# Optimization experiments

Measured on AMD Instinct MI355X. Metric: run time of the kernel, lower is better.

Reference implementation:

```python
import jax, jax.numpy as jnp
import numpy as np

# dims
B, L, IN, H, OUT = 2, 2048, 128, 512, 64
NL, ED, N, DR, K = 2, 1024, 16, 32, 4  # n_layers, d_inner=2*H, d_state, dt_rank=ceil(H/16), d_conv


def setup_inputs() -> dict:
    key = jax.random.key(0)
    ks = jax.random.split(key, 18)
    r = lambda k, s: 0.05 * jax.random.normal(k, s, dtype=jnp.float32)
    return {
        "x": jax.random.normal(ks[0], (B, L, IN), dtype=jnp.float32),
        # LiquidNet proj (in_dim -> hidden -> hidden)
        "p_Wi": r(ks[1], (IN, H)), "p_bi": r(ks[2], (H,)), "p_bh": r(ks[3], (H,)),
        "p_Wo": r(ks[4], (H, H)), "p_bo": r(ks[5], (H,)),
        # Mamba layers (stacked over layer axis)
        "m_norm_w": jnp.ones((NL, H), jnp.float32),
        "m_in_W": r(ks[6], (NL, H, 2 * ED)),
        "m_conv_w": r(ks[7], (NL, ED, K)), "m_conv_b": r(ks[8], (NL, ED)),
        "m_xproj_W": r(ks[9], (NL, ED, DR + 2 * N)),
        "m_dt_W": r(ks[10], (NL, DR, ED)), "m_dt_b": r(ks[11], (NL, ED)),
        "m_A_log": jnp.tile(jnp.log(jnp.arange(1, N + 1, dtype=jnp.float32)), (NL, ED, 1)),
        "m_D": jnp.ones((NL, ED), jnp.float32),
        "m_out_W": r(ks[12], (NL, ED, H)),
        # LiquidNet dense (hidden -> out_dim -> out_dim)
        "d_Wi": r(ks[13], (H, OUT)), "d_bi": r(ks[14], (OUT,)), "d_bh": r(ks[15], (OUT,)),
        "d_Wo": r(ks[16], (OUT, OUT)), "d_bo": r(ks[17], (OUT,)),
    }


def _rmsnorm(x, w, eps=1e-5):
    return x * jax.lax.rsqrt(jnp.mean(x * x, axis=-1, keepdims=True) + eps) * w


def _liquid(x, Wi, bi, bh, Wo, bo):
    # liquid cell with zero initial hidden state: h = tanh(i2h(x) + h2h(0))
    h = jnp.tanh(x @ Wi + bi + bh)
    return h @ Wo + bo


def _causal_conv(x, w, b):
    # x: [B, L, ED]; depthwise causal conv with kernel K
    xt = x.transpose(0, 2, 1)  # [B, ED, L]
    y = jax.lax.conv_general_dilated(xt, w[:, None, :], (1,), [(K - 1, 0)],
                                     dimension_numbers=('NCH', 'OIH', 'NCH'),
                                     feature_group_count=ED)
    return (y + b[None, :, None]).transpose(0, 2, 1)


def _ssm(xc, delta, Bm, Cm, A, D):
    # xc/delta: [B,L,ED]; Bm/Cm: [B,L,N]; A: [ED,N]; D: [ED]
    deltaA = jnp.exp(delta[..., None] * A)                              # [B,L,ED,N]
    deltaBx = delta[..., None] * Bm[:, :, None, :] * xc[..., None]      # [B,L,ED,N]

    def step(h, t):
        dA, dBx, Ct = t
        h = dA * h + dBx
        return h, jnp.einsum('bdn,bn->bd', h, Ct)

    h0 = jnp.zeros((xc.shape[0], ED, N), xc.dtype)
    _, ys = jax.lax.scan(step, h0, (deltaA.transpose(1, 0, 2, 3),
                                    deltaBx.transpose(1, 0, 2, 3),
                                    Cm.transpose(1, 0, 2)))
    return ys.transpose(1, 0, 2) + D * xc


def _mamba_block(x, norm_w, in_W, conv_w, conv_b, xproj_W, dt_W, dt_b, A_log, D, out_W):
    xn = _rmsnorm(x, norm_w)
    xz = xn @ in_W                       # [B,L,2*ED]
    xc, z = jnp.split(xz, 2, axis=-1)
    xc = jax.nn.silu(_causal_conv(xc, conv_w, conv_b))
    dbl = xc @ xproj_W                   # [B,L,DR+2N]
    dt, Bm, Cm = dbl[..., :DR], dbl[..., DR:DR + N], dbl[..., DR + N:]
    delta = jax.nn.softplus(dt @ dt_W + dt_b)
    y = _ssm(xc, delta, Bm, Cm, -jnp.exp(A_log), D)
    y = y * jax.nn.silu(z)
    return y @ out_W


def reference(x, p_Wi, p_bi, p_bh, p_Wo, p_bo,
              m_norm_w, m_in_W, m_conv_w, m_conv_b, m_xproj_W, m_dt_W, m_dt_b,
              m_A_log, m_D, m_out_W,
              d_Wi, d_bi, d_bh, d_Wo, d_bo):
    out = _liquid(x, p_Wi, p_bi, p_bh, p_Wo, p_bo)
    for l in range(NL):  # residual Mamba blocks
        out = out + _mamba_block(out, m_norm_w[l], m_in_W[l], m_conv_w[l], m_conv_b[l],
                                 m_xproj_W[l], m_dt_W[l], m_dt_b[l], m_A_log[l], m_D[l], m_out_W[l])
    out = _liquid(out, d_Wi, d_bi, d_bh, d_Wo, d_bo)
    out = out - jnp.tanh(out)  # Tanhshrink
    return out.reshape(-1)
```

## Files before the change

### kernel.cpp

```cpp
#include <hip/hip_runtime.h>
#include <hip/hip_bf16.h>
#include <cstdint>
#include <cstddef>

#define B_   2
#define L_   2048
#define IN_  128
#define H_   512
#define OUT_ 64
#define NL_  2
#define ED_  1024
#define N_   16
#define DR_  32
#define K_   4

static constexpr int M_TOK = B_ * L_;
static constexpr int SEG   = 64;
static constexpr int TS    = L_ / SEG;

typedef __attribute__((ext_vector_type(8))) short bhalf8;
typedef __attribute__((ext_vector_type(4))) float floatx4;

__device__ __forceinline__ void gld_lds16(const ushort* g, ushort* l)
{
    __builtin_amdgcn_global_load_lds(
        (const __attribute__((address_space(1))) unsigned int*)g,
        (__attribute__((address_space(3))) unsigned int*)l, 16, 0, 0);
}

template<int BM, int BN, int BK, int EPI, bool DUAL>
__global__ __launch_bounds__(256)
void mfma_gemm(const ushort* __restrict__ A, int lda,
               const ushort* Bt, int ldb,
               const ushort* Bt2, float* C2,
               const float* __restrict__ b1, const float* __restrict__ b2,
               float* C, __hip_bfloat16* Cb, int ldc,
               int M, int N, int kc)
{
    __shared__ __align__(16) ushort As[BM * BK];
    __shared__ __align__(16) ushort Bs[BN * BK];

    const int tid  = threadIdx.x;
    const int bm   = blockIdx.x * BM, bn = blockIdx.y * BN;
    int kz = 0, kbeg = 0;
    if (DUAL) {
        if (blockIdx.z) { Bt = Bt2; C = C2; }
    } else {
        kz = blockIdx.z; kbeg = kz * kc;
    }
    const int lane = tid & 63, wave = tid >> 6;
    const int wr = wave >> 1, wc = wave & 1;
    constexpr int WM = BM / 2, WN = BN / 2;
    constexpr int FM = WM / 16, FN = WN / 16;
    const int fr = lane & 15, fg = lane >> 4;

    constexpr int ACH = BM * BK / 512;
    constexpr int BCH = BN * BK / 512;
    constexpr int RPC = 512 / BK;
    constexpr int LPR = BK / 8;
    const int sr = lane / LPR;
    const int sc = (lane % LPR) * 8;

    floatx4 acc[FM][FN] = {};

    for (int k0 = kbeg; k0 < kbeg + kc; k0 += BK) {
        #pragma unroll
        for (int i = 0; i < ACH / 4; ++i) {
            const int ci = wave * (ACH / 4) + i;
            const int r  = ci * RPC + sr;
            gld_lds16(&A[(size_t)(bm + r) * lda + k0 + sc], &As[ci * 512]);
        }
        #pragma unroll
        for (int i = 0; i < BCH / 4; ++i) {
            const int ci = wave * (BCH / 4) + i;
            const int r  = ci * RPC + sr;
            gld_lds16(&Bt[(size_t)(bn + r) * ldb + k0 + sc], &Bs[ci * 512]);
        }
        __syncthreads();
        #pragma unroll
        for (int kk = 0; kk < BK; kk += 32) {
            bhalf8 fa[FM], fb[FN];
            #pragma unroll
            for (int m = 0; m < FM; ++m)
                fa[m] = *reinterpret_cast<const bhalf8*>(
                    &As[(wr * WM + m * 16 + fr) * BK + kk + fg * 8]);
            #pragma unroll
            for (int n = 0; n < FN; ++n)
                fb[n] = *reinterpret_cast<const bhalf8*>(
                    &Bs[(wc * WN + n * 16 + fr) * BK + kk + fg * 8]);
            #pragma unroll
            for (int m = 0; m < FM; ++m)
                #pragma unroll
                for (int n = 0; n < FN; ++n)
                    acc[m][n] = __builtin_amdgcn_mfma_f32_16x16x32_bf16(
                        fa[m], fb[n], acc[m][n], 0, 0, 0);
        }
        __syncthreads();
    }

    #pragma unroll
    for (int m = 0; m < FM; ++m) {
        #pragma unroll
        for (int n = 0; n < FN; ++n) {
            const int row0 = bm + wr * WM + m * 16 + fg * 4;
            const int col  = bn + wc * WN + n * 16 + fr;
            #pragma unroll
            for (int r = 0; r < 4; ++r) {
                float v = acc[m][n][r];
                const int row = row0 + r;
                if (EPI == 0) {
                    C[(size_t)row * ldc + col] = v;
                } else if (EPI == 1) {
                    C[(size_t)row * ldc + col] += v;
                } else if (EPI == 2) {
                    Cb[(size_t)row * ldc + col] =
                        __float2bfloat16(tanhf(v + b1[col] + b2[col]));
                } else if (EPI == 3) {
                    C[(size_t)row * ldc + col] = v + b1[col];
                } else if (EPI == 4) {
                    C[(size_t)kz * M * N + (size_t)row * N + col] = v;
                } else if (EPI == 5) {
                    const float w = v + b1[col];
                    C[(size_t)row * ldc + col] = w - tanhf(w);
                } else if (EPI == 6) {
                    const float w = v + b1[col];
                    C[(size_t)row * ldc + col] =
                        fmaxf(w, 0.0f) + log1pf(expf(-fabsf(w)));
                }
            }
        }
    }
}

template<int NP, int ACT, bool B1, bool B2, int OUTMODE>
__global__ __launch_bounds__(256)
void reduce_part_k(const float* __restrict__ P, const float* __restrict__ b1,
                   const float* __restrict__ b2, float* __restrict__ Of,
                   __hip_bfloat16* __restrict__ Ob, int MN, int Ncols)
{
    const int i = blockIdx.x * 256 + threadIdx.x;
    float s = 0.0f;
    #pragma unroll
    for (int z = 0; z < NP; ++z) s += P[(size_t)z * MN + i];
    const int col = i & (Ncols - 1);
    if (B1) s += b1[col];
    if (B2) s += b2[col];
    if (ACT == 1) s = tanhf(s);
    if (OUTMODE == 0 || OUTMODE == 2) Of[i] = s;
    if (OUTMODE == 1 || OUTMODE == 2) Ob[i] = __float2bfloat16(s);
}

__global__ __launch_bounds__(256)
void transpose_bf16_k(const float* __restrict__ W, __hip_bfloat16* __restrict__ Wt,
                      int K, int N)
{
    __shared__ float t[32][33];
    const int k0 = blockIdx.x * 32, n0 = blockIdx.y * 32;
    const int c = threadIdx.x & 31, r4 = threadIdx.x >> 5;
    #pragma unroll
    for (int i = 0; i < 4; ++i) {
        int r = r4 + i * 8;
        t[r][c] = W[(size_t)(k0 + r) * N + n0 + c];
    }
    __syncthreads();
    #pragma unroll
    for (int i = 0; i < 4; ++i) {
        int r = r4 + i * 8;
        Wt[(size_t)(n0 + r) * K + k0 + c] = __float2bfloat16(t[c][r]);
    }
}

__global__ __launch_bounds__(256)
void cvt_bf16_k(const float* __restrict__ in, __hip_bfloat16* __restrict__ out, int n)
{
    const int i = blockIdx.x * 256 + threadIdx.x;
    if (i < n) out[i] = __float2bfloat16(in[i]);
}

__global__ __launch_bounds__(256)
void rmsnorm_k(const float* __restrict__ x, const float* __restrict__ w,
               __hip_bfloat16* __restrict__ o)
{
    const int row = blockIdx.x;
    const int tid = threadIdx.x;
    const float* xr = x + (size_t)row * H_;
    float v0 = xr[tid], v1 = xr[tid + 256];
    float s = v0 * v0 + v1 * v1;
    #pragma unroll
    for (int off = 32; off > 0; off >>= 1) s += __shfl_down(s, off, 64);
    __shared__ float ps[4];
    __shared__ float scale_s;
    const int wave = tid >> 6, lane = tid & 63;
    if (lane == 0) ps[wave] = s;
    __syncthreads();
    if (tid == 0) {
        float tot = ps[0] + ps[1] + ps[2] + ps[3];
        scale_s = rsqrtf(tot * (1.0f / H_) + 1e-5f);
    }
    __syncthreads();
    const float sc = scale_s;
    o[(size_t)row * H_ + tid]       = __float2bfloat16(v0 * sc * w[tid]);
    o[(size_t)row * H_ + tid + 256] = __float2bfloat16(v1 * sc * w[tid + 256]);
}

__global__ __launch_bounds__(256)
void conv_silu_k(const float* __restrict__ xcr, const float* __restrict__ cw,
                 const float* __restrict__ cb, float* __restrict__ xc,
                 __hip_bfloat16* __restrict__ xcb)
{
    const int idx = blockIdx.x * 256 + threadIdx.x;
    const int d = idx & (ED_ - 1);
    const int t = (idx >> 10) & (L_ - 1);
    const int b = idx >> 21;
    const size_t base = (size_t)(b * L_ + t) * ED_ + d;
    float4 w = *reinterpret_cast<const float4*>(&cw[d * 4]);
    float acc = cb[d];
    acc += w.w * xcr[base];
    if (t >= 1) acc += w.z * xcr[base - 1 * ED_];
    if (t >= 2) acc += w.y * xcr[base - 2 * ED_];
    if (t >= 3) acc += w.x * xcr[base - 3 * ED_];
    const float s = acc / (1.0f + __expf(-acc));
    xc[base] = s;
    xcb[base] = __float2bfloat16(s);
}

template<bool P3>
__global__ __launch_bounds__(256)
void ssm_scan_k(const float* __restrict__ delta,
                const float* __restrict__ xc,
                const float* __restrict__ dbl,
                const float* __restrict__ zbuf,
                const float* __restrict__ A_log,
                const float* __restrict__ Dv,
                float* __restrict__ hend, float* __restrict__ pprod,
                const float* __restrict__ hinit,
                __hip_bfloat16* __restrict__ ybuf)
{
    __shared__ float bc[TS][32];
    const int bx   = blockIdx.x;
    const int seg  = bx & (SEG - 1);
    const int dblk = (bx >> 6) & 3;
    const int b    = bx >> 8;
    const int tid  = threadIdx.x;
    const int d    = dblk * 256 + tid;
    const size_t row0 = (size_t)(b * L_ + seg * TS);

    #pragma unroll
    for (int e = 0; e < (TS * 32) / 256; ++e) {
        int lin = tid + e * 256;
        bc[lin >> 5][lin & 31] = dbl[(row0 + (lin >> 5)) * 64 + 32 + (lin & 31)];
    }
    __syncthreads();

    float Av[N_];
    #pragma unroll
    for (int n = 0; n < N_; ++n) Av[n] = -expf(A_log[d * N_ + n]);

    float dv[TS], xv[TS];
    #pragma unroll
    for (int tt = 0; tt < TS; ++tt) dv[tt] = delta[(row0 + tt) * ED_ + d];
    #pragma unroll
    for (int tt = 0; tt < TS; ++tt) xv[tt] = xc[(row0 + tt) * ED_ + d];

    float h[N_], P[N_];
    if (P3) {
        #pragma unroll
        for (int n = 0; n < N_; ++n)
            h[n] = hinit[((size_t)(b * SEG + seg) * N_ + n) * ED_ + d];
    } else {
        #pragma unroll
        for (int n = 0; n < N_; ++n) { h[n] = 0.0f; P[n] = 1.0f; }
    }
    const float Dd = P3 ? Dv[d] : 0.0f;

    #pragma unroll
    for (int tt = 0; tt < TS; ++tt) {
        const float dvt = dv[tt];
        const float dx  = dvt * xv[tt];
        float ysum = 0.0f;
        #pragma unroll
        for (int n = 0; n < N_; ++n) {
            const float dA = __expf(dvt * Av[n]);
            h[n] = fmaf(dA, h[n], dx * bc[tt][n]);
            if (!P3) P[n] *= dA;
            else     ysum = fmaf(h[n], bc[tt][16 + n], ysum);
        }
        if (P3) {
            const float zv = zbuf[(row0 + tt) * ED_ + d];
            const float sz = zv / (1.0f + __expf(-zv));
            ybuf[(row0 + tt) * ED_ + d] =
                __float2bfloat16((ysum + Dd * xv[tt]) * sz);
        }
    }

    if (!P3) {
        #pragma unroll
        for (int n = 0; n < N_; ++n) {
            const size_t o = ((size_t)(b * SEG + seg) * N_ + n) * ED_ + d;
            hend[o]  = h[n];
            pprod[o] = P[n];
        }
    }
}

__global__ __launch_bounds__(256)
void ssm_combine_k(const float* __restrict__ hend, const float* __restrict__ pprod,
                   float* __restrict__ hinit)
{
    const int gid = blockIdx.x * 256 + threadIdx.x;
    const int d = gid & (ED_ - 1);
    const int n = (gid >> 10) & (N_ - 1);
    const int b = gid >> 14;
    size_t o = ((size_t)(b * SEG) * N_ + n) * ED_ + d;
    const size_t stride = (size_t)N_ * ED_;
    float h = 0.0f;
    #pragma unroll 8
    for (int s = 0; s < SEG; ++s) {
        hinit[o] = h;
        h = fmaf(pprod[o], h, hend[o]);
        o += stride;
    }
}

extern "C" void kernel_launch(void* const* d_in, const int* in_sizes, int n_in,
                              void* d_out, int out_size, void* d_ws, size_t ws_size,
                              hipStream_t stream)
{
    const float* x      = (const float*)d_in[0];
    const float* p_Wi   = (const float*)d_in[1];
    const float* p_bi   = (const float*)d_in[2];
    const float* p_bh   = (const float*)d_in[3];
    const float* p_Wo   = (const float*)d_in[4];
    const float* p_bo   = (const float*)d_in[5];
    const float* m_norm = (const float*)d_in[6];
    const float* m_inW  = (const float*)d_in[7];
    const float* m_cw   = (const float*)d_in[8];
    const float* m_cb   = (const float*)d_in[9];
    const float* m_xpW  = (const float*)d_in[10];
    const float* m_dtW  = (const float*)d_in[11];
    const float* m_dtb  = (const float*)d_in[12];
    const float* m_Alog = (const float*)d_in[13];
    const float* m_D    = (const float*)d_in[14];
    const float* m_outW = (const float*)d_in[15];
    const float* d_Wi   = (const float*)d_in[16];
    const float* d_bi   = (const float*)d_in[17];
    const float* d_bh   = (const float*)d_in[18];
    const float* d_Wo   = (const float*)d_in[19];
    const float* d_bo   = (const float*)d_in[20];
    float* out_f = (float*)d_out;
    float* ws = (float*)d_ws;

    float* OUT   = ws;
    float* XCR   = ws + 2097152;
    float* Z     = ws + 6291456;
    float* XC    = ws + 10485760;
    float* DBL   = ws + 14680064;
    float* DELTA = ws + 14942208;
    float* HINIT = ws + 19136512;
    float* BF    = ws + 21233664;
    float* WT    = ws + 23330816;
    float* DBLF  = ws + 25184256;

    float* HEND   = XCR;
    float* PPROD  = XCR + 2097152;
    float* CPARTX = DELTA;
    float* CPART2 = XCR;
    __hip_bfloat16* Xb   = (__hip_bfloat16*)BF;
    __hip_bfloat16* H1b  = (__hip_bfloat16*)(BF + 262144);
    __hip_bfloat16* XNb  = (__hip_bfloat16*)BF;
    __hip_bfloat16* XCb  = (__hip_bfloat16*)BF;
    __hip_bfloat16* YB   = (__hip_bfloat16*)BF;
    __hip_bfloat16* H2b  = (__hip_bfloat16*)BF;
    __hip_bfloat16* OUTb = (__hip_bfloat16*)XC;
    __hip_bfloat16* DBLb = (__hip_bfloat16*)DBLF;

    __hip_bfloat16* WTu     = (__hip_bfloat16*)WT;
    __hip_bfloat16* T_pWi   = WTu;
    __hip_bfloat16* T_pWo   = WTu + 65536;
    __hip_bfloat16* T_inW0  = WTu + 327680;
    __hip_bfloat16* T_inW1  = WTu + 1376256;
    __hip_bfloat16* T_xpW0  = WTu + 2424832;
    __hip_bfloat16* T_xpW1  = WTu + 2490368;
    __hip_bfloat16* T_outW0 = WTu + 2555904;
    __hip_bfloat16* T_outW1 = WTu + 3080192;
    __hip_bfloat16* T_dWi   = WTu + 3604480;
    __hip_bfloat16* T_dtW0  = WTu + 3637248;
    __hip_bfloat16* T_dtW1  = WTu + 3670016;
    __hip_bfloat16* T_dWo   = WTu + 3702784;

    const dim3 blk(256);

    cvt_bf16_k<<<dim3(2048), blk, 0, stream>>>(x, Xb, M_TOK * IN_);
    transpose_bf16_k<<<dim3(4, 16), blk, 0, stream>>>(p_Wi, T_pWi, IN_, H_);
    transpose_bf16_k<<<dim3(16, 16), blk, 0, stream>>>(p_Wo, T_pWo, H_, H_);
    transpose_bf16_k<<<dim3(16, 64), blk, 0, stream>>>(m_inW, T_inW0, H_, 2 * ED_);
    transpose_bf16_k<<<dim3(16, 64), blk, 0, stream>>>(m_inW + (size_t)H_ * 2 * ED_, T_inW1, H_, 2 * ED_);
    transpose_bf16_k<<<dim3(32, 2), blk, 0, stream>>>(m_xpW, T_xpW0, ED_, 64);
    transpose_bf16_k<<<dim3(32, 2), blk, 0, stream>>>(m_xpW + (size_t)ED_ * 64, T_xpW1, ED_, 64);
    transpose_bf16_k<<<dim3(32, 16), blk, 0, stream>>>(m_outW, T_outW0, ED_, H_);
    transpose_bf16_k<<<dim3(32, 16), blk, 0, stream>>>(m_outW + (size_t)ED_ * H_, T_outW1, ED_, H_);
    transpose_bf16_k<<<dim3(16, 2), blk, 0, stream>>>(d_Wi, T_dWi, H_, OUT_);
    transpose_bf16_k<<<dim3(1, 32), blk, 0, stream>>>(m_dtW, T_dtW0, DR_, ED_);
    transpose_bf16_k<<<dim3(1, 32), blk, 0, stream>>>(m_dtW + DR_ * ED_, T_dtW1, DR_, ED_);
    transpose_bf16_k<<<dim3(2, 2), blk, 0, stream>>>(d_Wo, T_dWo, OUT_, OUT_);

    mfma_gemm<128, 64, 64, 2, false><<<dim3(32, 8), blk, 0, stream>>>(
        (const ushort*)Xb, IN_, (const ushort*)T_pWi, IN_, nullptr, nullptr,
        p_bi, p_bh, nullptr, H1b, H_, M_TOK, H_, IN_);
    mfma_gemm<128, 64, 64, 3, false><<<dim3(32, 8), blk, 0, stream>>>(
        (const ushort*)H1b, H_, (const ushort*)T_pWo, H_, nullptr, nullptr,
        p_bo, nullptr, OUT, nullptr, H_, M_TOK, H_, H_);

    for (int l = 0; l < NL_; ++l) {
        const float* nw   = m_norm + l * H_;
        const float* cw   = m_cw   + l * ED_ * K_;
        const float* cb   = m_cb   + l * ED_;
        const float* dtb  = m_dtb  + l * ED_;
        const float* Alog = m_Alog + l * ED_ * N_;
        const float* Dv   = m_D    + l * ED_;
        const __hip_bfloat16* TinW  = l ? T_inW1  : T_inW0;
        const __hip_bfloat16* TxpW  = l ? T_xpW1  : T_xpW0;
        const __hip_bfloat16* ToutW = l ? T_outW1 : T_outW0;
        const __hip_bfloat16* TdtW  = l ? T_dtW1  : T_dtW0;

        rmsnorm_k<<<dim3(M_TOK), blk, 0, stream>>>(OUT, nw, XNb);
        mfma_gemm<128, 128, 64, 0, true><<<dim3(32, 8, 2), blk, 0, stream>>>(
            (const ushort*)XNb, H_, (const ushort*)TinW, H_,
            (const ushort*)(TinW + (size_t)ED_ * H_), Z,
            nullptr, nullptr, XCR, nullptr, ED_, M_TOK, ED_, H_);
        conv_silu_k<<<dim3(M_TOK * ED_ / 256), blk, 0, stream>>>(XCR, cw, cb, XC, XCb);
        mfma_gemm<128, 64, 64, 4, false><<<dim3(32, 1, 8), blk, 0, stream>>>(
            (const ushort*)XCb, ED_, (const ushort*)TxpW, ED_, nullptr, nullptr,
            nullptr, nullptr, CPARTX, nullptr, 64, M_TOK, 64, ED_ / 8);
        reduce_part_k<8, 0, false, false, 2><<<dim3(1024), blk, 0, stream>>>(
            CPARTX, nullptr, nullptr, DBL, DBLb, M_TOK * 64, 64);
        mfma_gemm<128, 64, 32, 6, false><<<dim3(32, 16), blk, 0, stream>>>(
            (const ushort*)DBLb, 64, (const ushort*)TdtW, DR_, nullptr, nullptr,
            dtb, nullptr, DELTA, nullptr, ED_, M_TOK, ED_, DR_);
        ssm_scan_k<false><<<dim3(512), blk, 0, stream>>>(
            DELTA, XC, DBL, nullptr, Alog, nullptr, HEND, PPROD, nullptr, nullptr);
        ssm_combine_k<<<dim3(128), blk, 0, stream>>>(HEND, PPROD, HINIT);
        ssm_scan_k<true><<<dim3(512), blk, 0, stream>>>(
            DELTA, XC, DBL, Z, Alog, Dv, nullptr, nullptr, HINIT, YB);
        mfma_gemm<128, 64, 64, 1, false><<<dim3(32, 8), blk, 0, stream>>>(
            (const ushort*)YB, ED_, (const ushort*)ToutW, ED_, nullptr, nullptr,
            nullptr, nullptr, OUT, nullptr, H_, M_TOK, H_, ED_);
    }

    cvt_bf16_k<<<dim3(8192), blk, 0, stream>>>(OUT, OUTb, M_TOK * H_);
    mfma_gemm<128, 64, 64, 4, false><<<dim3(32, 1, 8), blk, 0, stream>>>(
        (const ushort*)OUTb, H_, (const ushort*)T_dWi, H_, nullptr, nullptr,
        nullptr, nullptr, CPART2, nullptr, 64, M_TOK, 64, H_ / 8);
    reduce_part_k<8, 1, true, true, 1><<<dim3(1024), blk, 0, stream>>>(
        CPART2, d_bi, d_bh, nullptr, H2b, M_TOK * 64, 64);
    mfma_gemm<128, 64, 64, 5, false><<<dim3(32, 1), blk, 0, stream>>>(
        (const ushort*)H2b, OUT_, (const ushort*)T_dWo, OUT_, nullptr, nullptr,
        d_bo, nullptr, out_f, nullptr, OUT_, M_TOK, OUT_, OUT_);
}
```

Before: 358.4 us.

## Merge prep kernels, vectorize conv, split SSM state across lanes, fuse bf16 cast

Merges the input conversion and thirteen weight-transpose launches into one prep kernel. Vectorizes the causal conv+SiLU kernel to four channels per thread. Restructures the SSM scan so four lanes share each channel, each holding four states, with delta and xc staged in LDS and y reduced by shuffles; this quadruples the block count and lowers register pressure. The final out-projection writes the bf16 copy in its epilogue, removing the separate conversion kernel.

```diff
diff --git a/kernel.cpp b/kernel.cpp
--- a/kernel.cpp
+++ b/kernel.cpp
@@ -20,6 +20,12 @@
 
 typedef __attribute__((ext_vector_type(8))) short bhalf8;
 typedef __attribute__((ext_vector_type(4))) float floatx4;
+
+__device__ __forceinline__ ushort bf16bits(float f)
+{
+    __hip_bfloat16 h = __float2bfloat16(f);
+    return *reinterpret_cast<ushort*>(&h);
+}
 
 __device__ __forceinline__ void gld_lds16(const ushort* g, ushort* l)
 {
@@ -126,6 +132,11 @@
                     const float w = v + b1[col];
                     C[(size_t)row * ldc + col] =
                         fmaxf(w, 0.0f) + log1pf(expf(-fabsf(w)));
+                } else if (EPI == 7) {
+                    float* cp = C + (size_t)row * ldc + col;
+                    const float w = *cp + v;
+                    *cp = w;
+                    Cb[(size_t)row * ldc + col] = __float2bfloat16(w);
                 }
             }
         }
@@ -150,32 +161,66 @@
     if (OUTMODE == 1 || OUTMODE == 2) Ob[i] = __float2bfloat16(s);
 }
 
-__global__ __launch_bounds__(256)
-void transpose_bf16_k(const float* __restrict__ W, __hip_bfloat16* __restrict__ Wt,
-                      int K, int N)
+__device__ __forceinline__ void tr32(float (*t)[33],
+                                     const float* __restrict__ W,
+                                     __hip_bfloat16* __restrict__ Wt,
+                                     int K, int N, int local, int gx, int tid)
+{
+    const int kx = local % gx, ny = local / gx;
+    const int k0 = kx * 32, n0 = ny * 32;
+    const int c = tid & 31, r4 = tid >> 5;
+    #pragma unroll
+    for (int i = 0; i < 4; ++i) {
+        const int rr = r4 + i * 8;
+        t[rr][c] = W[(size_t)(k0 + rr) * N + n0 + c];
+    }
+    __syncthreads();
+    #pragma unroll
+    for (int i = 0; i < 4; ++i) {
+        const int rr = r4 + i * 8;
+        Wt[(size_t)(n0 + rr) * K + k0 + c] = __float2bfloat16(t[c][rr]);
+    }
+}
+
+__global__ __launch_bounds__(256)
+void prep_k(const float* __restrict__ x, __hip_bfloat16* __restrict__ Xb,
+            const float* pWi, __hip_bfloat16* TpWi,
+            const float* pWo, __hip_bfloat16* TpWo,
+            const float* inW, __hip_bfloat16* TinW0, __hip_bfloat16* TinW1,
+            const float* xpW, __hip_bfloat16* TxpW0, __hip_bfloat16* TxpW1,
+            const float* outW, __hip_bfloat16* ToutW0, __hip_bfloat16* ToutW1,
+            const float* dWi, __hip_bfloat16* TdWi,
+            const float* dtW, __hip_bfloat16* TdtW0, __hip_bfloat16* TdtW1,
+            const float* dWo, __hip_bfloat16* TdWo)
 {
     __shared__ float t[32][33];
-    const int k0 = blockIdx.x * 32, n0 = blockIdx.y * 32;
-    const int c = threadIdx.x & 31, r4 = threadIdx.x >> 5;
-    #pragma unroll
-    for (int i = 0; i < 4; ++i) {
-        int r = r4 + i * 8;
-        t[r][c] = W[(size_t)(k0 + r) * N + n0 + c];
-    }
-    __syncthreads();
-    #pragma unroll
-    for (int i = 0; i < 4; ++i) {
-        int r = r4 + i * 8;
-        Wt[(size_t)(n0 + r) * K + k0 + c] = __float2bfloat16(t[c][r]);
-    }
-}
-
-__global__ __launch_bounds__(256)
-void cvt_bf16_k(const float* __restrict__ in, __hip_bfloat16* __restrict__ out, int n)
-{
-    const int i = blockIdx.x * 256 + threadIdx.x;
-    if (i < n) out[i] = __float2bfloat16(in[i]);
-}
+    const int tid = threadIdx.x;
+    int r = blockIdx.x;
+
+    if (r < 512) {
+        const int i = (r * 256 + tid) * 4;
+        const float4 v = *reinterpret_cast<const float4*>(&x[i]);
+        ushort4 u;
+        u.x = bf16bits(v.x); u.y = bf16bits(v.y);
+        u.z = bf16bits(v.z); u.w = bf16bits(v.w);
+        *reinterpret_cast<ushort4*>(&Xb[i]) = u;
+        return;
+    }
+    r -= 512;
+    if (r < 64)   { tr32(t, pWi, TpWi, IN_, H_, r, 4, tid); return; }   r -= 64;
+    if (r < 256)  { tr32(t, pWo, TpWo, H_, H_, r, 16, tid); return; }   r -= 256;
+    if (r < 1024) { tr32(t, inW, TinW0, H_, 2 * ED_, r, 16, tid); return; } r -= 1024;
+    if (r < 1024) { tr32(t, inW + (size_t)H_ * 2 * ED_, TinW1, H_, 2 * ED_, r, 16, tid); return; } r -= 1024;
+    if (r < 64)   { tr32(t, xpW, TxpW0, ED_, 64, r, 32, tid); return; } r -= 64;
+    if (r < 64)   { tr32(t, xpW + (size_t)ED_ * 64, TxpW1, ED_, 64, r, 32, tid); return; } r -= 64;
+    if (r < 512)  { tr32(t, outW, ToutW0, ED_, H_, r, 32, tid); return; } r -= 512;
+    if (r < 512)  { tr32(t, outW + (size_t)ED_ * H_, ToutW1, ED_, H_, r, 32, tid); return; } r -= 512;
+    if (r < 32)   { tr32(t, dWi, TdWi, H_, OUT_, r, 16, tid); return; } r -= 32;
+    if (r < 32)   { tr32(t, dtW, TdtW0, DR_, ED_, r, 1, tid); return; } r -= 32;
+    if (r < 32)   { tr32(t, dtW + DR_ * ED_, TdtW1, DR_, ED_, r, 1, tid); return; } r -= 32;
+    tr32(t, dWo, TdWo, OUT_, OUT_, r, 2, tid);
+}
+static constexpr int PREP_BLOCKS = 512 + 64 + 256 + 1024 + 1024 + 64 + 64 + 512 + 512 + 32 + 32 + 32 + 4;
 
 __global__ __launch_bounds__(256)
 void rmsnorm_k(const float* __restrict__ x, const float* __restrict__ w,
@@ -209,19 +254,34 @@
                  __hip_bfloat16* __restrict__ xcb)
 {
     const int idx = blockIdx.x * 256 + threadIdx.x;
-    const int d = idx & (ED_ - 1);
-    const int t = (idx >> 10) & (L_ - 1);
-    const int b = idx >> 21;
-    const size_t base = (size_t)(b * L_ + t) * ED_ + d;
-    float4 w = *reinterpret_cast<const float4*>(&cw[d * 4]);
-    float acc = cb[d];
-    acc += w.w * xcr[base];
-    if (t >= 1) acc += w.z * xcr[base - 1 * ED_];
-    if (t >= 2) acc += w.y * xcr[base - 2 * ED_];
-    if (t >= 3) acc += w.x * xcr[base - 3 * ED_];
-    const float s = acc / (1.0f + __expf(-acc));
-    xc[base] = s;
-    xcb[base] = __float2bfloat16(s);
+    const int d4 = (idx & (ED_ / 4 - 1)) * 4;
+    const int t  = (idx >> 8) & (L_ - 1);
+    const int b  = idx >> 19;
+    const size_t base = (size_t)(b * L_ + t) * ED_ + d4;
+
+    float4 x0 = *reinterpret_cast<const float4*>(&xcr[base]);
+    float4 x1 = {}, x2 = {}, x3 = {};
+    if (t >= 1) x1 = *reinterpret_cast<const float4*>(&xcr[base - 1 * ED_]);
+    if (t >= 2) x2 = *reinterpret_cast<const float4*>(&xcr[base - 2 * ED_]);
+    if (t >= 3) x3 = *reinterpret_cast<const float4*>(&xcr[base - 3 * ED_]);
+    const float4 bias = *reinterpret_cast<const float4*>(&cb[d4]);
+
+    float4 out;
+    ushort4 outb;
+    #pragma unroll
+    for (int j = 0; j < 4; ++j) {
+        const float4 w = *reinterpret_cast<const float4*>(&cw[(d4 + j) * 4]);
+        float acc = (&bias.x)[j];
+        acc += w.w * (&x0.x)[j];
+        acc += w.z * (&x1.x)[j];
+        acc += w.y * (&x2.x)[j];
+        acc += w.x * (&x3.x)[j];
+        const float s = acc / (1.0f + __expf(-acc));
+        (&out.x)[j] = s;
+        (&outb.x)[j] = bf16bits(s);
+    }
+    *reinterpret_cast<float4*>(&xc[base]) = out;
+    *reinterpret_cast<ushort4*>(&xcb[base]) = outb;
 }
 
 template<bool P3>
@@ -236,69 +296,83 @@
                 const float* __restrict__ hinit,
                 __hip_bfloat16* __restrict__ ybuf)
 {
+    __shared__ float sdl[TS][64];
+    __shared__ float sxc[TS][64];
     __shared__ float bc[TS][32];
     const int bx   = blockIdx.x;
     const int seg  = bx & (SEG - 1);
-    const int dblk = (bx >> 6) & 3;
-    const int b    = bx >> 8;
+    const int dblk = (bx >> 6) & 15;
+    const int b    = bx >> 10;
     const int tid  = threadIdx.x;
-    const int d    = dblk * 256 + tid;
+    const int dl   = tid >> 2;
+    const int ng   = tid & 3;
+    const int d    = dblk * 64 + dl;
+    const int dbase = dblk * 64;
     const size_t row0 = (size_t)(b * L_ + seg * TS);
 
     #pragma unroll
-    for (int e = 0; e < (TS * 32) / 256; ++e) {
-        int lin = tid + e * 256;
+    for (int e = 0; e < 8; ++e) {
+        const int lin = tid + e * 256;
+        sdl[lin >> 6][lin & 63] = delta[(row0 + (lin >> 6)) * ED_ + dbase + (lin & 63)];
+    }
+    #pragma unroll
+    for (int e = 0; e < 8; ++e) {
+        const int lin = tid + e * 256;
+        sxc[lin >> 6][lin & 63] = xc[(row0 + (lin >> 6)) * ED_ + dbase + (lin & 63)];
+    }
+    #pragma unroll
+    for (int e = 0; e < 4; ++e) {
+        const int lin = tid + e * 256;
         bc[lin >> 5][lin & 31] = dbl[(row0 + (lin >> 5)) * 64 + 32 + (lin & 31)];
     }
+
+    float Av[4];
+    #pragma unroll
+    for (int i = 0; i < 4; ++i) Av[i] = -expf(A_log[d * N_ + ng * 4 + i]);
+
+    float h[4], P[4];
+    if (P3) {
+        #pragma unroll
+        for (int i = 0; i < 4; ++i)
+            h[i] = hinit[((size_t)(b * SEG + seg) * N_ + ng * 4 + i) * ED_ + d];
+    } else {
+        #pragma unroll
+        for (int i = 0; i < 4; ++i) { h[i] = 0.0f; P[i] = 1.0f; }
+    }
+    const float Dd = P3 ? Dv[d] : 0.0f;
     __syncthreads();
 
-    float Av[N_];
-    #pragma unroll
-    for (int n = 0; n < N_; ++n) Av[n] = -expf(A_log[d * N_ + n]);
-
-    float dv[TS], xv[TS];
-    #pragma unroll
-    for (int tt = 0; tt < TS; ++tt) dv[tt] = delta[(row0 + tt) * ED_ + d];
-    #pragma unroll
-    for (int tt = 0; tt < TS; ++tt) xv[tt] = xc[(row0 + tt) * ED_ + d];
-
-    float h[N_], P[N_];
-    if (P3) {
-        #pragma unroll
-        for (int n = 0; n < N_; ++n)
-            h[n] = hinit[((size_t)(b * SEG + seg) * N_ + n) * ED_ + d];
-    } else {
-        #pragma unroll
-        for (int n = 0; n < N_; ++n) { h[n] = 0.0f; P[n] = 1.0f; }
-    }
-    const float Dd = P3 ? Dv[d] : 0.0f;
-
-    #pragma unroll
-    for (int tt = 0; tt < TS; ++tt) {
-        const float dvt = dv[tt];
-        const float dx  = dvt * xv[tt];
+    #pragma unroll
+    for (int t = 0; t < TS; ++t) {
+        const float dvt = sdl[t][dl];
+        const float xvt = sxc[t][dl];
+        const float dx  = dvt * xvt;
         float ysum = 0.0f;
         #pragma unroll
-        for (int n = 0; n < N_; ++n) {
-            const float dA = __expf(dvt * Av[n]);
-            h[n] = fmaf(dA, h[n], dx * bc[tt][n]);
-            if (!P3) P[n] *= dA;
-            else     ysum = fmaf(h[n], bc[tt][16 + n], ysum);
+        for (int i = 0; i < 4; ++i) {
+            const float dA = __expf(dvt * Av[i]);
+            h[i] = fmaf(dA, h[i], dx * bc[t][ng * 4 + i]);
+            if (!P3) P[i] *= dA;
+            else     ysum = fmaf(h[i], bc[t][16 + ng * 4 + i], ysum);
         }
         if (P3) {
-            const float zv = zbuf[(row0 + tt) * ED_ + d];
-            const float sz = zv / (1.0f + __expf(-zv));
-            ybuf[(row0 + tt) * ED_ + d] =
-                __float2bfloat16((ysum + Dd * xv[tt]) * sz);
+            float y2 = ysum + __shfl_xor(ysum, 1, 64);
+            float y4 = y2 + __shfl_xor(y2, 2, 64);
+            if (ng == 0) {
+                const float zv = zbuf[(row0 + t) * ED_ + d];
+                const float sz = zv / (1.0f + __expf(-zv));
+                ybuf[(row0 + t) * ED_ + d] =
+                    __float2bfloat16((y4 + Dd * xvt) * sz);
+            }
         }
     }
 
     if (!P3) {
         #pragma unroll
-        for (int n = 0; n < N_; ++n) {
-            const size_t o = ((size_t)(b * SEG + seg) * N_ + n) * ED_ + d;
-            hend[o]  = h[n];
-            pprod[o] = P[n];
+        for (int i = 0; i < 4; ++i) {
+            const size_t o = ((size_t)(b * SEG + seg) * N_ + ng * 4 + i) * ED_ + d;
+            hend[o]  = h[i];
+            pprod[o] = P[i];
         }
     }
 }
@@ -390,19 +464,10 @@
 
     const dim3 blk(256);
 
-    cvt_bf16_k<<<dim3(2048), blk, 0, stream>>>(x, Xb, M_TOK * IN_);
-    transpose_bf16_k<<<dim3(4, 16), blk, 0, stream>>>(p_Wi, T_pWi, IN_, H_);
-    transpose_bf16_k<<<dim3(16, 16), blk, 0, stream>>>(p_Wo, T_pWo, H_, H_);
-    transpose_bf16_k<<<dim3(16, 64), blk, 0, stream>>>(m_inW, T_inW0, H_, 2 * ED_);
-    transpose_bf16_k<<<dim3(16, 64), blk, 0, stream>>>(m_inW + (size_t)H_ * 2 * ED_, T_inW1, H_, 2 * ED_);
-    transpose_bf16_k<<<dim3(32, 2), blk, 0, stream>>>(m_xpW, T_xpW0, ED_, 64);
-    transpose_bf16_k<<<dim3(32, 2), blk, 0, stream>>>(m_xpW + (size_t)ED_ * 64, T_xpW1, ED_, 64);
-    transpose_bf16_k<<<dim3(32, 16), blk, 0, stream>>>(m_outW, T_outW0, ED_, H_);
-    transpose_bf16_k<<<dim3(32, 16), blk, 0, stream>>>(m_outW + (size_t)ED_ * H_, T_outW1, ED_, H_);
-    transpose_bf16_k<<<dim3(16, 2), blk, 0, stream>>>(d_Wi, T_dWi, H_, OUT_);
-    transpose_bf16_k<<<dim3(1, 32), blk, 0, stream>>>(m_dtW, T_dtW0, DR_, ED_);
-    transpose_bf16_k<<<dim3(1, 32), blk, 0, stream>>>(m_dtW + DR_ * ED_, T_dtW1, DR_, ED_);
-    transpose_bf16_k<<<dim3(2, 2), blk, 0, stream>>>(d_Wo, T_dWo, OUT_, OUT_);
+    prep_k<<<dim3(PREP_BLOCKS), blk, 0, stream>>>(
+        x, Xb, p_Wi, T_pWi, p_Wo, T_pWo, m_inW, T_inW0, T_inW1,
+        m_xpW, T_xpW0, T_xpW1, m_outW, T_outW0, T_outW1,
+        d_Wi, T_dWi, m_dtW, T_dtW0, T_dtW1, d_Wo, T_dWo);
 
     mfma_gemm<128, 64, 64, 2, false><<<dim3(32, 8), blk, 0, stream>>>(
         (const ushort*)Xb, IN_, (const ushort*)T_pWi, IN_, nullptr, nullptr,
@@ -428,7 +493,7 @@
             (const ushort*)XNb, H_, (const ushort*)TinW, H_,
             (const ushort*)(TinW + (size_t)ED_ * H_), Z,
             nullptr, nullptr, XCR, nullptr, ED_, M_TOK, ED_, H_);
-        conv_silu_k<<<dim3(M_TOK * ED_ / 256), blk, 0, stream>>>(XCR, cw, cb, XC, XCb);
+        conv_silu_k<<<dim3(M_TOK * ED_ / 4 / 256), blk, 0, stream>>>(XCR, cw, cb, XC, XCb);
         mfma_gemm<128, 64, 64, 4, false><<<dim3(32, 1, 8), blk, 0, stream>>>(
             (const ushort*)XCb, ED_, (const ushort*)TxpW, ED_, nullptr, nullptr,
             nullptr, nullptr, CPARTX, nullptr, 64, M_TOK, 64, ED_ / 8);
@@ -437,17 +502,22 @@
         mfma_gemm<128, 64, 32, 6, false><<<dim3(32, 16), blk, 0, stream>>>(
             (const ushort*)DBLb, 64, (const ushort*)TdtW, DR_, nullptr, nullptr,
             dtb, nullptr, DELTA, nullptr, ED_, M_TOK, ED_, DR_);
-        ssm_scan_k<false><<<dim3(512), blk, 0, stream>>>(
+        ssm_scan_k<false><<<dim3(2048), blk, 0, stream>>>(
             DELTA, XC, DBL, nullptr, Alog, nullptr, HEND, PPROD, nullptr, nullptr);
         ssm_combine_k<<<dim3(128), blk, 0, stream>>>(HEND, PPROD, HINIT);
-        ssm_scan_k<true><<<dim3(512), blk, 0, stream>>>(
+        ssm_scan_k<true><<<dim3(2048), blk, 0, stream>>>(
             DELTA, XC, DBL, Z, Alog, Dv, nullptr, nullptr, HINIT, YB);
-        mfma_gemm<128, 64, 64, 1, false><<<dim3(32, 8), blk, 0, stream>>>(
-            (const ushort*)YB, ED_, (const ushort*)ToutW, ED_, nullptr, nullptr,
-            nullptr, nullptr, OUT, nullptr, H_, M_TOK, H_, ED_);
-    }
-
-    cvt_bf16_k<<<dim3(8192), blk, 0, stream>>>(OUT, OUTb, M_TOK * H_);
+        if (l == 0) {
+            mfma_gemm<128, 64, 64, 1, false><<<dim3(32, 8), blk, 0, stream>>>(
+                (const ushort*)YB, ED_, (const ushort*)ToutW, ED_, nullptr, nullptr,
+                nullptr, nullptr, OUT, nullptr, H_, M_TOK, H_, ED_);
+        } else {
+            mfma_gemm<128, 64, 64, 7, false><<<dim3(32, 8), blk, 0, stream>>>(
+                (const ushort*)YB, ED_, (const ushort*)ToutW, ED_, nullptr, nullptr,
+                nullptr, nullptr, OUT, OUTb, H_, M_TOK, H_, ED_);
+        }
+    }
+
     mfma_gemm<128, 64, 64, 4, false><<<dim3(32, 1, 8), blk, 0, stream>>>(
         (const ushort*)OUTb, H_, (const ushort*)T_dWi, H_, nullptr, nullptr,
         nullptr, nullptr, CPART2, nullptr, 64, M_TOK, 64, H_ / 8);
```

Result: faster. 342.5 us (-4.4%).
